# Kernel optimization log

Measured on AMD Instinct MI355X. Metric: run time of the kernel, lower is better.

## Reference

```python
import jax
import jax.numpy as jnp
import numpy as np

T, M, N = 8192, 1024, 2048

def setup_inputs() -> dict:
    key = jax.random.key(0)
    k1, k2, k3, k4, k5 = jax.random.split(key, 5)
    s = 1.0 / np.sqrt(N)  # PyTorch RNN default init scale (uniform +-1/sqrt(n)); randn*s keeps magnitudes sane
    return {
        "X_in": jax.random.normal(k1, (T, M), dtype=jnp.float32),
        "W_ih": jax.random.normal(k2, (N, M), dtype=jnp.float32) * s,
        "W_hh": jax.random.normal(k3, (N, N), dtype=jnp.float32) * s,
        "b_ih": jax.random.normal(k4, (N,), dtype=jnp.float32) * s,
        "b_hh": jax.random.normal(k5, (N,), dtype=jnp.float32) * s,
    }

def reference(X_in, W_ih, W_hh, b_ih, b_hh):
    # h_t = tanh(W_ih x_t + b_ih + W_hh h_{t-1} + b_hh); Y[t] = h_t, h_0 = 0.
    # Input projection is recurrence-free: batch it as one big GEMM.
    pre = X_in @ W_ih.T + (b_ih + b_hh)  # (T, N)
    h0 = jnp.zeros((N,), dtype=X_in.dtype)

    def step(h, p):
        h_new = jnp.tanh(p + W_hh @ h)
        return h_new, h_new

    _, Y = jax.lax.scan(step, h0, pre)  # Y: (T, N)
    return Y
```

## Files before the change

### kernel.cpp

```cpp
#include <hip/hip_runtime.h>
#include <hip/hip_bf16.h>
#include <math.h>

#define T_STEPS 8192
#define M_DIM   1024
#define N_DIM   2048

typedef unsigned long long u64;

__global__ __launch_bounds__(256) void pre_gemm(
    const float* __restrict__ X, const float* __restrict__ Wih,
    const float* __restrict__ bih, const float* __restrict__ bhh,
    float* __restrict__ out)
{
  __shared__ float As[128][36];
  __shared__ float Bs[128][36];
  const int tid = threadIdx.x;
  const int tx = tid & 15;
  const int ty = tid >> 4;
  const int bt = blockIdx.x * 128;
  const int bn = blockIdx.y * 128;

  float acc[8][8];
  #pragma unroll
  for (int i = 0; i < 8; ++i)
    #pragma unroll
    for (int j = 0; j < 8; ++j) acc[i][j] = 0.f;

  for (int k0 = 0; k0 < M_DIM; k0 += 32) {
    #pragma unroll
    for (int s = 0; s < 4; ++s) {
      int slot = tid + s * 256;
      int row  = slot >> 3;
      int c4   = (slot & 7) << 2;
      float4 va = *(const float4*)&X  [(size_t)(bt + row) * M_DIM + k0 + c4];
      float4 vb = *(const float4*)&Wih[(size_t)(bn + row) * M_DIM + k0 + c4];
      *(float4*)&As[row][c4] = va;
      *(float4*)&Bs[row][c4] = vb;
    }
    __syncthreads();
    #pragma unroll
    for (int kk = 0; kk < 32; kk += 4) {
      float4 a4[8], b4[8];
      #pragma unroll
      for (int i = 0; i < 8; ++i) a4[i] = *(const float4*)&As[ty + 16 * i][kk];
      #pragma unroll
      for (int j = 0; j < 8; ++j) b4[j] = *(const float4*)&Bs[tx + 16 * j][kk];
      #pragma unroll
      for (int i = 0; i < 8; ++i)
        #pragma unroll
        for (int j = 0; j < 8; ++j) {
          acc[i][j] = fmaf(a4[i].x, b4[j].x, acc[i][j]);
          acc[i][j] = fmaf(a4[i].y, b4[j].y, acc[i][j]);
          acc[i][j] = fmaf(a4[i].z, b4[j].z, acc[i][j]);
          acc[i][j] = fmaf(a4[i].w, b4[j].w, acc[i][j]);
        }
    }
    __syncthreads();
  }

  float bsum[8];
  #pragma unroll
  for (int j = 0; j < 8; ++j) {
    int col = bn + tx + 16 * j;
    bsum[j] = bih[col] + bhh[col];
  }
  #pragma unroll
  for (int i = 0; i < 8; ++i) {
    int rowg = bt + ty + 16 * i;
    #pragma unroll
    for (int j = 0; j < 8; ++j)
      out[(size_t)rowg * N_DIM + bn + tx + 16 * j] = acc[i][j] + bsum[j];
  }
}

__global__ __launch_bounds__(256) void rnn_persist(
    const float* __restrict__ Whh,
    float* __restrict__ Y,
    u64* __restrict__ hbuf)
{
  __shared__ float h_lds[N_DIM];
  const int tid  = threadIdx.x;
  const int b    = blockIdx.x;
  const int r    = tid >> 5;
  const int c    = tid & 31;
  const int grow = b * 8 + r;

  float w[64];
  #pragma unroll
  for (int k = 0; k < 64; ++k)
    w[k] = Whh[(size_t)grow * N_DIM + c + 32 * k];

  for (int t = 0; t < T_STEPS; ++t) {
    float prev_pre = 0.f;
    if (c == 0) prev_pre = Y[(size_t)t * N_DIM + grow];

    u64* __restrict__ src = hbuf + (t & 1) * N_DIM;
    u64* __restrict__ dst = hbuf + ((t + 1) & 1) * N_DIM;
    const unsigned need = (unsigned)t;

    float hv[8];
    unsigned pending = 0xffu;
    while (pending) {
      #pragma unroll
      for (int i = 0; i < 8; ++i)
        if (pending & (1u << i)) {
          u64 p = __hip_atomic_load(&src[tid + 256 * i], __ATOMIC_RELAXED,
                                    __HIP_MEMORY_SCOPE_AGENT);
          if ((unsigned)(p >> 32) >= need) {
            hv[i] = __uint_as_float((unsigned)(p & 0xffffffffu));
            pending &= ~(1u << i);
          }
        }
    }
    #pragma unroll
    for (int i = 0; i < 8; ++i) h_lds[tid + 256 * i] = hv[i];
    __syncthreads();

    float acc = 0.f;
    #pragma unroll
    for (int k = 0; k < 64; ++k)
      acc = fmaf(w[k], h_lds[c + 32 * k], acc);

    #pragma unroll
    for (int off = 16; off >= 1; off >>= 1)
      acc += __shfl_xor(acc, off, 64);

    if (c == 0) {
      float hn = tanhf(acc + prev_pre);
      __hip_atomic_store(&Y[(size_t)t * N_DIM + grow], hn, __ATOMIC_RELAXED,
                         __HIP_MEMORY_SCOPE_AGENT);
      u64 pk = ((u64)(unsigned)(t + 1) << 32) | (u64)__float_as_uint(hn);
      __hip_atomic_store(&dst[grow], pk, __ATOMIC_RELAXED,
                         __HIP_MEMORY_SCOPE_AGENT);
    }
    __syncthreads();
  }
}

extern "C" void kernel_launch(void* const* d_in, const int* in_sizes, int n_in,
                              void* d_out, int out_size, void* d_ws, size_t ws_size,
                              hipStream_t stream) {
  const float* X   = (const float*)d_in[0];
  const float* Wih = (const float*)d_in[1];
  const float* Whh = (const float*)d_in[2];
  const float* bih = (const float*)d_in[3];
  const float* bhh = (const float*)d_in[4];
  float* Y = (float*)d_out;

  u64* hbuf = (u64*)d_ws;

  hipMemsetAsync(d_ws, 0, 2 * N_DIM * sizeof(u64), stream);

  dim3 gA(T_STEPS / 128, N_DIM / 128);
  pre_gemm<<<gA, dim3(256), 0, stream>>>(X, Wih, bih, bhh, Y);

  rnn_persist<<<dim3(256), dim3(256), 0, stream>>>(Whh, Y, hbuf);
}
```

Before: 35.47 ms.

## Replace per-element tagged h polling with per-block flags and coalesced Y rows

The persistent RNN kernel no longer packs a step tag with every hidden-state value. Each block now publishes its 8 values plus a single per-block flag, and readers poll 256 flags before loading the hidden vector as 64-bit pairs. This cuts the cross-block polling traffic and the size of each spin. Output rows are no longer written by scattered per-element atomic stores: one rotating block writes the whole previous h row coalesced, and block 0 writes the final row. The price is an extra __syncthreads per step, and correctness now depends on the flag/data ordering built from relaxed atomics plus an s_waitcnt.

```diff
diff --git a/kernel.cpp b/kernel.cpp
--- a/kernel.cpp
+++ b/kernel.cpp
@@ -7,6 +7,7 @@
 #define N_DIM   2048
 
 typedef unsigned long long u64;
+typedef unsigned int u32;
 
 __global__ __launch_bounds__(256) void pre_gemm(
     const float* __restrict__ X, const float* __restrict__ Wih,
@@ -77,14 +78,17 @@
 __global__ __launch_bounds__(256) void rnn_persist(
     const float* __restrict__ Whh,
     float* __restrict__ Y,
-    u64* __restrict__ hbuf)
+    float* __restrict__ hdata,
+    u32* __restrict__ flags)
 {
   __shared__ float h_lds[N_DIM];
+  __shared__ float hstage[8];
   const int tid  = threadIdx.x;
   const int b    = blockIdx.x;
   const int r    = tid >> 5;
   const int c    = tid & 31;
   const int grow = b * 8 + r;
+  const int f0   = tid >> 2;
 
   float w[64];
   #pragma unroll
@@ -92,49 +96,91 @@
     w[k] = Whh[(size_t)grow * N_DIM + c + 32 * k];
 
   for (int t = 0; t < T_STEPS; ++t) {
+    const int p = t & 1;
+
     float prev_pre = 0.f;
     if (c == 0) prev_pre = Y[(size_t)t * N_DIM + grow];
 
-    u64* __restrict__ src = hbuf + (t & 1) * N_DIM;
-    u64* __restrict__ dst = hbuf + ((t + 1) & 1) * N_DIM;
-    const unsigned need = (unsigned)t;
-
-    float hv[8];
-    unsigned pending = 0xffu;
-    while (pending) {
-      #pragma unroll
-      for (int i = 0; i < 8; ++i)
-        if (pending & (1u << i)) {
-          u64 p = __hip_atomic_load(&src[tid + 256 * i], __ATOMIC_RELAXED,
-                                    __HIP_MEMORY_SCOPE_AGENT);
-          if ((unsigned)(p >> 32) >= need) {
-            hv[i] = __uint_as_float((unsigned)(p & 0xffffffffu));
-            pending &= ~(1u << i);
+    u64 hd[4];
+    const u64* hsrc = (const u64*)(hdata + p * N_DIM);
+    {
+      const u32 need = (u32)t;
+      unsigned pend = 0xFu;
+      while (pend) {
+        #pragma unroll
+        for (int i = 0; i < 4; ++i)
+          if (pend & (1u << i)) {
+            u32 v = __hip_atomic_load(&flags[p * 256 + f0 + 64 * i],
+                                      __ATOMIC_RELAXED, __HIP_MEMORY_SCOPE_AGENT);
+            if (v >= need) {
+              asm volatile("" ::: "memory");
+              hd[i] = __hip_atomic_load(&hsrc[tid + 256 * i],
+                                        __ATOMIC_RELAXED, __HIP_MEMORY_SCOPE_AGENT);
+              pend &= ~(1u << i);
+            }
+          }
+      }
+    }
+    #pragma unroll
+    for (int i = 0; i < 4; ++i)
+      ((u64*)h_lds)[tid + 256 * i] = hd[i];
+    __syncthreads();
+
+    float acc = 0.f;
+    #pragma unroll
+    for (int k = 0; k < 64; ++k)
+      acc = fmaf(w[k], h_lds[c + 32 * k], acc);
+    #pragma unroll
+    for (int off = 16; off >= 1; off >>= 1)
+      acc += __shfl_xor(acc, off, 64);
+
+    if (b == (t & 255) && t > 0) {
+      u64* yrow = (u64*)(Y + (size_t)(t - 1) * N_DIM);
+      #pragma unroll
+      for (int i = 0; i < 4; ++i)
+        yrow[tid + 256 * i] = hd[i];
+    }
+
+    if (c == 0) {
+      float hn = tanhf(acc + prev_pre);
+      hstage[r] = hn;
+    }
+    __syncthreads();
+
+    if (tid < 8) {
+      float v = hstage[tid];
+      __hip_atomic_store(&hdata[((t + 1) & 1) * N_DIM + b * 8 + tid], v,
+                         __ATOMIC_RELAXED, __HIP_MEMORY_SCOPE_AGENT);
+      asm volatile("s_waitcnt vmcnt(0)" ::: "memory");
+      if (tid == 0)
+        __hip_atomic_store(&flags[((t + 1) & 1) * 256 + b], (u32)(t + 1),
+                           __ATOMIC_RELAXED, __HIP_MEMORY_SCOPE_AGENT);
+    }
+  }
+
+  if (b == 0) {
+    const u32 need = (u32)T_STEPS;
+    unsigned pend = 0xFu;
+    u64 hd[4];
+    const u64* hsrc = (const u64*)(hdata + 0 * N_DIM);
+    while (pend) {
+      #pragma unroll
+      for (int i = 0; i < 4; ++i)
+        if (pend & (1u << i)) {
+          u32 v = __hip_atomic_load(&flags[0 * 256 + f0 + 64 * i],
+                                    __ATOMIC_RELAXED, __HIP_MEMORY_SCOPE_AGENT);
+          if (v >= need) {
+            asm volatile("" ::: "memory");
+            hd[i] = __hip_atomic_load(&hsrc[tid + 256 * i],
+                                      __ATOMIC_RELAXED, __HIP_MEMORY_SCOPE_AGENT);
+            pend &= ~(1u << i);
           }
         }
     }
-    #pragma unroll
-    for (int i = 0; i < 8; ++i) h_lds[tid + 256 * i] = hv[i];
-    __syncthreads();
-
-    float acc = 0.f;
-    #pragma unroll
-    for (int k = 0; k < 64; ++k)
-      acc = fmaf(w[k], h_lds[c + 32 * k], acc);
-
-    #pragma unroll
-    for (int off = 16; off >= 1; off >>= 1)
-      acc += __shfl_xor(acc, off, 64);
-
-    if (c == 0) {
-      float hn = tanhf(acc + prev_pre);
-      __hip_atomic_store(&Y[(size_t)t * N_DIM + grow], hn, __ATOMIC_RELAXED,
-                         __HIP_MEMORY_SCOPE_AGENT);
-      u64 pk = ((u64)(unsigned)(t + 1) << 32) | (u64)__float_as_uint(hn);
-      __hip_atomic_store(&dst[grow], pk, __ATOMIC_RELAXED,
-                         __HIP_MEMORY_SCOPE_AGENT);
-    }
-    __syncthreads();
+    u64* yrow = (u64*)(Y + (size_t)(T_STEPS - 1) * N_DIM);
+    #pragma unroll
+    for (int i = 0; i < 4; ++i)
+      yrow[tid + 256 * i] = hd[i];
   }
 }
 
@@ -148,12 +194,13 @@
   const float* bhh = (const float*)d_in[4];
   float* Y = (float*)d_out;
 
-  u64* hbuf = (u64*)d_ws;
-
-  hipMemsetAsync(d_ws, 0, 2 * N_DIM * sizeof(u64), stream);
+  float* hdata = (float*)d_ws;
+  u32*   flags = (u32*)((char*)d_ws + 16384);
+
+  hipMemsetAsync(d_ws, 0, 16384 + 2048, stream);
 
   dim3 gA(T_STEPS / 128, N_DIM / 128);
   pre_gemm<<<gA, dim3(256), 0, stream>>>(X, Wih, bih, bhh, Y);
 
-  rnn_persist<<<dim3(256), dim3(256), 0, stream>>>(Whh, Y, hbuf);
+  rnn_persist<<<dim3(256), dim3(256), 0, stream>>>(Whh, Y, hdata, flags);
 }
```

After: 41.44 ms. 16.8% more time.

## Compute matvec directly on polled registers and defer Y writes round-robin

Applied to the files above, without the earlier changes.

Each thread now holds eight weights for each of the block's eight rows, aligned with the h elements it already polls from the global exchange buffer. This removes the LDS staging of the full h vector and one barrier. Partial sums go through a padded LDS reduction plus a wave shuffle. Y for step t-1 is written coalesced by one rotating block per step, instead of scattered per-row atomic stores, with a final tail write for the last step. The cost is an LDS transpose reduction and a second synchronization per step.

```diff
diff --git a/kernel.cpp b/kernel.cpp
--- a/kernel.cpp
+++ b/kernel.cpp
@@ -7,6 +7,7 @@
 #define N_DIM   2048
 
 typedef unsigned long long u64;
+typedef unsigned int u32;
 
 __global__ __launch_bounds__(256) void pre_gemm(
     const float* __restrict__ X, const float* __restrict__ Wih,
@@ -79,62 +80,98 @@
     float* __restrict__ Y,
     u64* __restrict__ hbuf)
 {
-  __shared__ float h_lds[N_DIM];
-  const int tid  = threadIdx.x;
-  const int b    = blockIdx.x;
-  const int r    = tid >> 5;
-  const int c    = tid & 31;
-  const int grow = b * 8 + r;
+  __shared__ float part[256 * 9];
+  const int tid = threadIdx.x;
+  const int b   = blockIdx.x;
+  const int r   = tid >> 5;
+  const int k   = tid & 31;
 
-  float w[64];
+  float wreg[8][8];
   #pragma unroll
-  for (int k = 0; k < 64; ++k)
-    w[k] = Whh[(size_t)grow * N_DIM + c + 32 * k];
+  for (int rr = 0; rr < 8; ++rr)
+    #pragma unroll
+    for (int i = 0; i < 8; ++i)
+      wreg[rr][i] = Whh[(size_t)(b * 8 + rr) * N_DIM + tid + 256 * i];
 
   for (int t = 0; t < T_STEPS; ++t) {
-    float prev_pre = 0.f;
-    if (c == 0) prev_pre = Y[(size_t)t * N_DIM + grow];
+    const int p = t & 1;
+    float ppre = 0.f;
+    if (k == 0) ppre = Y[(size_t)t * N_DIM + b * 8 + r];
 
-    u64* __restrict__ src = hbuf + (t & 1) * N_DIM;
-    u64* __restrict__ dst = hbuf + ((t + 1) & 1) * N_DIM;
-    const unsigned need = (unsigned)t;
+    const u64* __restrict__ src = hbuf + p * N_DIM;
+    u64* __restrict__ dst = hbuf + (p ^ 1) * N_DIM;
+    const u32 need = (u32)t;
 
     float hv[8];
-    unsigned pending = 0xffu;
-    while (pending) {
+    unsigned pend = 0xffu;
+    while (pend) {
       #pragma unroll
       for (int i = 0; i < 8; ++i)
-        if (pending & (1u << i)) {
-          u64 p = __hip_atomic_load(&src[tid + 256 * i], __ATOMIC_RELAXED,
-                                    __HIP_MEMORY_SCOPE_AGENT);
-          if ((unsigned)(p >> 32) >= need) {
-            hv[i] = __uint_as_float((unsigned)(p & 0xffffffffu));
-            pending &= ~(1u << i);
+        if (pend & (1u << i)) {
+          u64 pk = __hip_atomic_load(&src[tid + 256 * i], __ATOMIC_RELAXED,
+                                     __HIP_MEMORY_SCOPE_AGENT);
+          if ((u32)(pk >> 32) >= need) {
+            hv[i] = __uint_as_float((u32)pk);
+            pend &= ~(1u << i);
+          }
+        }
+    }
+
+    float acc[8];
+    #pragma unroll
+    for (int rr = 0; rr < 8; ++rr) {
+      float a = 0.f;
+      #pragma unroll
+      for (int i = 0; i < 8; ++i) a = fmaf(wreg[rr][i], hv[i], a);
+      acc[rr] = a;
+    }
+    #pragma unroll
+    for (int rr = 0; rr < 8; ++rr) part[tid * 9 + rr] = acc[rr];
+
+    if (t > 0 && b == (t & 255)) {
+      #pragma unroll
+      for (int i = 0; i < 8; ++i)
+        Y[(size_t)(t - 1) * N_DIM + tid + 256 * i] = hv[i];
+    }
+    __syncthreads();
+
+    float s = 0.f;
+    #pragma unroll
+    for (int j = 0; j < 8; ++j)
+      s += part[(k + 32 * j) * 9 + r];
+    #pragma unroll
+    for (int off = 16; off >= 1; off >>= 1)
+      s += __shfl_xor(s, off, 64);
+
+    if (k == 0) {
+      float hn = tanhf(s + ppre);
+      u64 pk = ((u64)(u32)(t + 1) << 32) | (u64)__float_as_uint(hn);
+      __hip_atomic_store(&dst[b * 8 + r], pk, __ATOMIC_RELAXED,
+                         __HIP_MEMORY_SCOPE_AGENT);
+    }
+    __syncthreads();
+  }
+
+  if (b == 0) {
+    const u32 need = (u32)T_STEPS;
+    const u64* __restrict__ src = hbuf;
+    float hv[8];
+    unsigned pend = 0xffu;
+    while (pend) {
+      #pragma unroll
+      for (int i = 0; i < 8; ++i)
+        if (pend & (1u << i)) {
+          u64 pk = __hip_atomic_load(&src[tid + 256 * i], __ATOMIC_RELAXED,
+                                     __HIP_MEMORY_SCOPE_AGENT);
+          if ((u32)(pk >> 32) >= need) {
+            hv[i] = __uint_as_float((u32)pk);
+            pend &= ~(1u << i);
           }
         }
     }
     #pragma unroll
-    for (int i = 0; i < 8; ++i) h_lds[tid + 256 * i] = hv[i];
-    __syncthreads();
-
-    float acc = 0.f;
-    #pragma unroll
-    for (int k = 0; k < 64; ++k)
-      acc = fmaf(w[k], h_lds[c + 32 * k], acc);
-
-    #pragma unroll
-    for (int off = 16; off >= 1; off >>= 1)
-      acc += __shfl_xor(acc, off, 64);
-
-    if (c == 0) {
-      float hn = tanhf(acc + prev_pre);
-      __hip_atomic_store(&Y[(size_t)t * N_DIM + grow], hn, __ATOMIC_RELAXED,
-                         __HIP_MEMORY_SCOPE_AGENT);
-      u64 pk = ((u64)(unsigned)(t + 1) << 32) | (u64)__float_as_uint(hn);
-      __hip_atomic_store(&dst[grow], pk, __ATOMIC_RELAXED,
-                         __HIP_MEMORY_SCOPE_AGENT);
-    }
-    __syncthreads();
+    for (int i = 0; i < 8; ++i)
+      Y[(size_t)(T_STEPS - 1) * N_DIM + tid + 256 * i] = hv[i];
   }
 }
 
```

After: 28.47 ms. -19.7%, faster.
